# Performance work log

Measured on AMD Instinct MI355X. Metric: run time of the kernel, lower is better.

Reference implementation:

```python
import jax, jax.numpy as jnp
import numpy as np


def setup_inputs() -> dict:
    key = jax.random.key(0)
    B, R, N, F = 8, 16, 6144, 128  # batch, rotations, gpc_systems (vertices), features
    inputs = jax.random.normal(key, (B, R, N, F), dtype=jnp.float32)
    return {"inputs": inputs}


def reference(inputs):
    # inputs: [B, R, N, F]
    # Euclidean norm over features -> [B, R, N]
    rotation_norms = jnp.linalg.norm(inputs, axis=-1)
    # winning rotation per (batch, gpc_system) -> [B, N]
    winner_rotation = jnp.argmax(rotation_norms, axis=1)
    # gather the winning rotation's feature vector: [B, N, F]
    out = jnp.take_along_axis(inputs, winner_rotation[:, None, :, None], axis=1)
    return out[:, 0]  # squeeze rotation axis
```

## Files before the change

kernel.cpp:

```cpp
#include <hip/hip_runtime.h>

#define BB 8
#define RR 16
#define NN 6144
#define FF 128

typedef float f32x4 __attribute__((ext_vector_type(4)));

__global__ __launch_bounds__(256, 8) void amp_kernel(const float* __restrict__ in,
                                                     float* __restrict__ out) {
    const int tid     = blockIdx.x * 256 + threadIdx.x;
    const int wave    = tid >> 6;
    const int lane    = tid & 63;
    const int quarter = lane >> 4;
    const int sublane = lane & 15;

    const int b     = wave / (NN / 4);
    const int n_grp = wave - b * (NN / 4);
    const int n     = n_grp * 4 + quarter;

    const size_t base    = (((size_t)b * RR) * NN + n) * (size_t)FF + (sublane << 2);
    const size_t rstride = (size_t)NN * FF;

    float best_sum = -1.f;
    int   best_r   = 0;

    const float* p = in + base;
    #pragma unroll 4
    for (int r = 0; r < RR; ++r) {
        const f32x4 va = *(const f32x4*)p;
        const f32x4 vb = *(const f32x4*)(p + 64);
        p += rstride;
        float s = va.x * va.x + va.y * va.y + va.z * va.z + va.w * va.w
                + vb.x * vb.x + vb.y * vb.y + vb.z * vb.z + vb.w * vb.w;
        s += __shfl_xor(s, 1);
        s += __shfl_xor(s, 2);
        s += __shfl_xor(s, 4);
        s += __shfl_xor(s, 8);
        if (s > best_sum) {
            best_sum = s;
            best_r   = r;
        }
    }

    const float* q = in + base + (size_t)best_r * rstride;
    const f32x4 wa = *(const f32x4*)q;
    const f32x4 wb = *(const f32x4*)(q + 64);

    float* o = out + ((size_t)b * NN + n) * (size_t)FF + (sublane << 2);
    __builtin_nontemporal_store(wa, (f32x4*)o);
    __builtin_nontemporal_store(wb, (f32x4*)(o + 64));
}

extern "C" void kernel_launch(void* const* d_in, const int* in_sizes, int n_in,
                              void* d_out, int out_size, void* d_ws, size_t ws_size,
                              hipStream_t stream) {
    const float* in  = (const float*)d_in[0];
    float*       out = (float*)d_out;

    const int n_waves  = BB * NN / 4;
    const int n_blocks = n_waves / 4;

    amp_kernel<<<dim3(n_blocks), dim3(256), 0, stream>>>(in, out);
}
```

Measured before the change: 523.4 us.

## Split into contiguous norm pass and argmax-gather pass via global norms buffer

Replaces the single kernel that strided across rotations per vector with two kernels: one streams the input contiguously computing per-row squared norms into a global buffer, the other does a cross-lane argmax over the 16 rotations and gathers the winning vector. The aim is fully sequential, high-parallelism reads instead of 16 widely strided accesses per wave. It adds a second launch, a small norms buffer round-trip, and a re-read of the winning rows.

```diff
diff --git a/kernel.cpp b/kernel.cpp
--- a/kernel.cpp
+++ b/kernel.cpp
@@ -7,7 +7,42 @@
 
 typedef float f32x4 __attribute__((ext_vector_type(4)));
 
-__global__ __launch_bounds__(256, 8) void amp_kernel(const float* __restrict__ in,
+__device__ float g_norms[(size_t)BB * NN * RR];
+
+#define P1_WAVES 12288
+#define P1_ITERS 16
+
+__global__ __launch_bounds__(256) void norm_kernel(const float* __restrict__ in) {
+    const int tid     = blockIdx.x * 256 + threadIdx.x;
+    const int wave    = tid >> 6;
+    const int lane    = tid & 63;
+    const int quarter = lane >> 4;
+    const int sublane = lane & 15;
+
+    #pragma unroll 4
+    for (int i = 0; i < P1_ITERS; ++i) {
+        const int chunk = wave + i * P1_WAVES;
+        const int g     = chunk * 4 + quarter;
+        const float* p  = in + (size_t)g * FF + (sublane << 2);
+        const f32x4 va  = *(const f32x4*)p;
+        const f32x4 vb  = *(const f32x4*)(p + 64);
+        float s = va.x * va.x + va.y * va.y + va.z * va.z + va.w * va.w
+                + vb.x * vb.x + vb.y * vb.y + vb.z * vb.z + vb.w * vb.w;
+        s += __shfl_xor(s, 1);
+        s += __shfl_xor(s, 2);
+        s += __shfl_xor(s, 4);
+        s += __shfl_xor(s, 8);
+        if (sublane == 0) {
+            const int n  = g % NN;
+            const int br = g / NN;
+            const int r  = br & (RR - 1);
+            const int b  = br >> 4;
+            g_norms[((size_t)(b * NN + n) << 4) + r] = s;
+        }
+    }
+}
+
+__global__ __launch_bounds__(256) void gather_kernel(const float* __restrict__ in,
                                                      float* __restrict__ out) {
     const int tid     = blockIdx.x * 256 + threadIdx.x;
     const int wave    = tid >> 6;
@@ -15,39 +50,27 @@
     const int quarter = lane >> 4;
     const int sublane = lane & 15;
 
-    const int b     = wave / (NN / 4);
-    const int n_grp = wave - b * (NN / 4);
-    const int n     = n_grp * 4 + quarter;
+    const int j = wave * 4 + quarter;
 
-    const size_t base    = (((size_t)b * RR) * NN + n) * (size_t)FF + (sublane << 2);
-    const size_t rstride = (size_t)NN * FF;
-
-    float best_sum = -1.f;
-    int   best_r   = 0;
-
-    const float* p = in + base;
-    #pragma unroll 4
-    for (int r = 0; r < RR; ++r) {
-        const f32x4 va = *(const f32x4*)p;
-        const f32x4 vb = *(const f32x4*)(p + 64);
-        p += rstride;
-        float s = va.x * va.x + va.y * va.y + va.z * va.z + va.w * va.w
-                + vb.x * vb.x + vb.y * vb.y + vb.z * vb.z + vb.w * vb.w;
-        s += __shfl_xor(s, 1);
-        s += __shfl_xor(s, 2);
-        s += __shfl_xor(s, 4);
-        s += __shfl_xor(s, 8);
-        if (s > best_sum) {
-            best_sum = s;
-            best_r   = r;
-        }
+    float s  = g_norms[((size_t)j << 4) + sublane];
+    int   idx = sublane;
+    #pragma unroll
+    for (int m = 1; m < 16; m <<= 1) {
+        const float so = __shfl_xor(s, m);
+        const int   io = __shfl_xor(idx, m);
+        const bool take = (so > s) || ((so == s) && (io < idx));
+        s   = take ? so : s;
+        idx = take ? io : idx;
     }
 
-    const float* q = in + base + (size_t)best_r * rstride;
+    const int b = j / NN;
+    const int n = j - b * NN;
+
+    const float* q = in + (((size_t)(b * RR + idx)) * NN + n) * (size_t)FF + (sublane << 2);
     const f32x4 wa = *(const f32x4*)q;
     const f32x4 wb = *(const f32x4*)(q + 64);
 
-    float* o = out + ((size_t)b * NN + n) * (size_t)FF + (sublane << 2);
+    float* o = out + (size_t)j * FF + (sublane << 2);
     __builtin_nontemporal_store(wa, (f32x4*)o);
     __builtin_nontemporal_store(wb, (f32x4*)(o + 64));
 }
@@ -58,8 +81,8 @@
     const float* in  = (const float*)d_in[0];
     float*       out = (float*)d_out;
 
-    const int n_waves  = BB * NN / 4;
-    const int n_blocks = n_waves / 4;
+    norm_kernel<<<dim3(P1_WAVES / 4), dim3(256), 0, stream>>>(in);
 
-    amp_kernel<<<dim3(n_blocks), dim3(256), 0, stream>>>(in, out);
+    const int p2_blocks = (BB * NN / 4) / 4;
+    gather_kernel<<<dim3(p2_blocks), dim3(256), 0, stream>>>(in, out);
 }
```

New measurement: 532.2 us. Within noise of the previous version (+1.7%).
